# Kernel optimization log

Measured on AMD Instinct MI355X. Metric: run time of the kernel, lower is better.

The kernel has to match this reference:

```python
import jax, jax.numpy as jnp
import numpy as np

B, D, O = 512, 512, 512  # batch, indim, outdim

def setup_inputs() -> dict:
    key = jax.random.key(0)
    k1, k2, k3 = jax.random.split(key, 3)
    x = jax.random.normal(k1, (B, D), dtype=jnp.float32)
    mu_weight = jax.random.normal(k2, (O, D), dtype=jnp.float32) / np.sqrt(D)
    # inverse diagonal covariance entries (positive in spirit; uniform fill)
    inv_diag_C_weight = jax.random.uniform(k3, (O, D), dtype=jnp.float32)
    return {"x": x, "mu_weight": mu_weight, "inv_diag_C_weight": inv_diag_C_weight}

def reference(x, mu_weight, inv_diag_C_weight):
    # Original: logits = -(x-mu) @ diag(invC) @ (x-mu)^T per (batch, class) pair.
    # Diagonal structure => elementwise squared diff weighted by invC, summed over D.
    diff = x[:, None, :] - mu_weight[None, :, :]            # [B, O, D]
    logits = -jnp.einsum('bod,od->bo', diff * diff, inv_diag_C_weight)
    return logits                                            # [B, O]
```

## Files before the change

kernel.cpp:

```cpp
#include <hip/hip_runtime.h>

#define B_DIM 512
#define D_DIM 512
#define O_DIM 512
#define KSPLIT 8
#define DCHUNK 64


__global__ __launch_bounds__(256, 2)
void gda_main(const float* __restrict__ x,
              const float* __restrict__ mu,
              const float* __restrict__ ic,
              float* __restrict__ ws) {
    __shared__ float4 lds_x4[64 * 16];
    __shared__ float4 lds_ab4[64 * 16 * 2];
    __shared__ float  lds_cp[64 * 16];
    __shared__ float  lds_c[64];

    const int tid = threadIdx.x;
    const int bid = blockIdx.x;
    const int bb = bid & 7, ob = (bid >> 3) & 7, ks = bid >> 6;
    const int b0 = bb * 64, o0 = ob * 64, d0 = ks * DCHUNK;

    const int g   = tid & 15;
    const int row = tid >> 4;
#pragma unroll
    for (int i = 0; i < 4; ++i) {
        const int r = row + 16 * i;
        const int sw = g ^ (r & 7);
        const float4 xv = *(const float4*)&x [(b0 + r) * D_DIM + d0 + g * 4];
        lds_x4[r * 16 + sw] = xv;
        const float4 m4 = *(const float4*)&mu[(o0 + r) * D_DIM + d0 + g * 4];
        const float4 c4 = *(const float4*)&ic[(o0 + r) * D_DIM + d0 + g * 4];
        float4 a4, b4;
        a4.x = -c4.x;            a4.y = -c4.y;
        a4.z = -c4.z;            a4.w = -c4.w;
        b4.x = 2.0f * m4.x * c4.x; b4.y = 2.0f * m4.y * c4.y;
        b4.z = 2.0f * m4.z * c4.z; b4.w = 2.0f * m4.w * c4.w;
        lds_ab4[(r * 16 + sw) * 2 + 0] = a4;
        lds_ab4[(r * 16 + sw) * 2 + 1] = b4;
        lds_cp[r * 16 + g] = m4.x * m4.x * c4.x + m4.y * m4.y * c4.y
                           + m4.z * m4.z * c4.z + m4.w * m4.w * c4.w;
    }
    __syncthreads();

    if (tid < 64) {
        float s = 0.0f;
#pragma unroll
        for (int q = 0; q < 16; ++q) s += lds_cp[tid * 16 + q];
        lds_c[tid] = -s;
    }

    const int w    = tid >> 6;
    const int lane = tid & 63;
    const int cb   = lane >> 3;
    const int r8   = lane & 7;
    const int wb   = (w & 1) * 32, wo = (w >> 1) * 32;

    float acc[16];
#pragma unroll
    for (int q = 0; q < 16; ++q) acc[q] = 0.0f;

#pragma unroll
    for (int gg = 0; gg < 16; ++gg) {
        float4 xr[4], xs[4];
#pragma unroll
        for (int k = 0; k < 4; ++k) {
            xr[k] = lds_x4[(wb + cb + 8 * k) * 16 + (gg ^ cb)];
            xs[k].x = xr[k].x * xr[k].x;
            xs[k].y = xr[k].y * xr[k].y;
            xs[k].z = xr[k].z * xr[k].z;
            xs[k].w = xr[k].w * xr[k].w;
        }
#pragma unroll
        for (int j = 0; j < 4; ++j) {
            const int oo = wo + r8 + 8 * j;
            const float4 a4 = lds_ab4[(oo * 16 + (gg ^ r8)) * 2 + 0];
            const float4 b4 = lds_ab4[(oo * 16 + (gg ^ r8)) * 2 + 1];
#pragma unroll
            for (int k = 0; k < 4; ++k) {
                float t = acc[k * 4 + j];
                t = fmaf(a4.x, xs[k].x, t);  t = fmaf(b4.x, xr[k].x, t);
                t = fmaf(a4.y, xs[k].y, t);  t = fmaf(b4.y, xr[k].y, t);
                t = fmaf(a4.z, xs[k].z, t);  t = fmaf(b4.z, xr[k].z, t);
                t = fmaf(a4.w, xs[k].w, t);  t = fmaf(b4.w, xr[k].w, t);
                acc[k * 4 + j] = t;
            }
        }
    }
    __syncthreads();

    float* wsb = (float*)ws + (size_t)bid * 4096;
#pragma unroll
    for (int j = 0; j < 4; ++j) {
        const float cc = lds_c[wo + r8 + 8 * j];
#pragma unroll
        for (int k = 0; k < 4; ++k)
            wsb[(wb + cb + 8 * k) * 64 + (wo + r8 + 8 * j)] = acc[k * 4 + j] + cc;
    }
}

__global__ __launch_bounds__(256, 4)
void gda_reduce(const float* __restrict__ ws, float* __restrict__ out) {
    const int t0 = blockIdx.x * 1024 + threadIdx.x;
#pragma unroll
    for (int p = 0; p < 4; ++p) {
        const int flat = t0 + p * 256;
        const int b = flat >> 9, o = flat & 511;
        const int bb = b >> 6, bl = b & 63, ob = o >> 6, ol = o & 63;
        const float* base = ws + ((ob * 8 + bb) * 4096 + bl * 64 + ol);
        float s = 0.0f;
#pragma unroll
        for (int k = 0; k < KSPLIT; ++k) s += base[k * (64 * 4096)];
        out[flat] = s;
    }
}

extern "C" void kernel_launch(void* const* d_in, const int* in_sizes, int n_in,
                              void* d_out, int out_size, void* d_ws, size_t ws_size,
                              hipStream_t stream) {
    const float* x  = (const float*)d_in[0];
    const float* mu = (const float*)d_in[1];
    const float* ic = (const float*)d_in[2];
    float* ws  = (float*)d_ws;
    float* out = (float*)d_out;

    gda_main  <<<dim3(512), dim3(256), 0, stream>>>(x, mu, ic, ws);
    gda_reduce<<<dim3(256), dim3(256), 0, stream>>>(ws, out);
}
```

Measured before the change: 74.03 us.

## Use 128x64 tiles with 16-way K split, padded LDS and Horner FMA

Reshapes the main kernel to 128-row batch tiles with half-width D chunks and a 16-way K split. Each thread now holds 32 accumulators, which increases register reuse of the loaded mu/ic coefficients. The squared-x precompute is replaced with a Horner-form FMA pair, and XOR swizzling is replaced by padded LDS rows. The reduce kernel is vectorized with float4 loads, but workspace traffic doubles because of the larger split.

After: 76.51 us. 1.03x slower.

```diff
diff --git a/kernel.cpp b/kernel.cpp
--- a/kernel.cpp
+++ b/kernel.cpp
@@ -3,8 +3,8 @@
 #define B_DIM 512
 #define D_DIM 512
 #define O_DIM 512
-#define KSPLIT 8
-#define DCHUNK 64
+#define KSPLIT 16
+#define DCHUNK 32
 
 
 __global__ __launch_bounds__(256, 2)
@@ -12,42 +12,45 @@
               const float* __restrict__ mu,
               const float* __restrict__ ic,
               float* __restrict__ ws) {
-    __shared__ float4 lds_x4[64 * 16];
-    __shared__ float4 lds_ab4[64 * 16 * 2];
-    __shared__ float  lds_cp[64 * 16];
+    __shared__ float4 lds_x[128 * 9];
+    __shared__ float4 lds_a[64 * 9];
+    __shared__ float4 lds_b[64 * 9];
+    __shared__ float  lds_cp[64 * 9];
     __shared__ float  lds_c[64];
 
     const int tid = threadIdx.x;
     const int bid = blockIdx.x;
-    const int bb = bid & 7, ob = (bid >> 3) & 7, ks = bid >> 6;
-    const int b0 = bb * 64, o0 = ob * 64, d0 = ks * DCHUNK;
+    const int bb = bid & 3, ob = (bid >> 2) & 7, ks = bid >> 5;
+    const int b0 = bb * 128, o0 = ob * 64, d0 = ks * DCHUNK;
 
-    const int g   = tid & 15;
-    const int row = tid >> 4;
+    const int g   = tid & 7;
+    const int row = tid >> 3;
 #pragma unroll
     for (int i = 0; i < 4; ++i) {
-        const int r = row + 16 * i;
-        const int sw = g ^ (r & 7);
-        const float4 xv = *(const float4*)&x [(b0 + r) * D_DIM + d0 + g * 4];
-        lds_x4[r * 16 + sw] = xv;
+        const int r = row + 32 * i;
+        lds_x[r * 9 + g] = *(const float4*)&x[(b0 + r) * D_DIM + d0 + g * 4];
+    }
+#pragma unroll
+    for (int i = 0; i < 2; ++i) {
+        const int r = row + 32 * i;
         const float4 m4 = *(const float4*)&mu[(o0 + r) * D_DIM + d0 + g * 4];
         const float4 c4 = *(const float4*)&ic[(o0 + r) * D_DIM + d0 + g * 4];
         float4 a4, b4;
-        a4.x = -c4.x;            a4.y = -c4.y;
-        a4.z = -c4.z;            a4.w = -c4.w;
+        a4.x = -c4.x;              a4.y = -c4.y;
+        a4.z = -c4.z;              a4.w = -c4.w;
         b4.x = 2.0f * m4.x * c4.x; b4.y = 2.0f * m4.y * c4.y;
         b4.z = 2.0f * m4.z * c4.z; b4.w = 2.0f * m4.w * c4.w;
-        lds_ab4[(r * 16 + sw) * 2 + 0] = a4;
-        lds_ab4[(r * 16 + sw) * 2 + 1] = b4;
-        lds_cp[r * 16 + g] = m4.x * m4.x * c4.x + m4.y * m4.y * c4.y
-                           + m4.z * m4.z * c4.z + m4.w * m4.w * c4.w;
+        lds_a[r * 9 + g] = a4;
+        lds_b[r * 9 + g] = b4;
+        lds_cp[r * 9 + g] = m4.x * m4.x * c4.x + m4.y * m4.y * c4.y
+                          + m4.z * m4.z * c4.z + m4.w * m4.w * c4.w;
     }
     __syncthreads();
 
     if (tid < 64) {
         float s = 0.0f;
 #pragma unroll
-        for (int q = 0; q < 16; ++q) s += lds_cp[tid * 16 + q];
+        for (int q = 0; q < 8; ++q) s += lds_cp[tid * 9 + q];
         lds_c[tid] = -s;
     }
 
@@ -55,65 +58,64 @@
     const int lane = tid & 63;
     const int cb   = lane >> 3;
     const int r8   = lane & 7;
-    const int wb   = (w & 1) * 32, wo = (w >> 1) * 32;
+    const int wb   = (w & 1) * 64, wo = (w >> 1) * 32;
 
-    float acc[16];
+    const float4* xb = &lds_x[(wb + cb) * 9];
+    const float4* ap = &lds_a[(wo + r8) * 9];
+    const float4* bp = &lds_b[(wo + r8) * 9];
+
+    float acc[32];
 #pragma unroll
-    for (int q = 0; q < 16; ++q) acc[q] = 0.0f;
+    for (int q = 0; q < 32; ++q) acc[q] = 0.0f;
 
 #pragma unroll
-    for (int gg = 0; gg < 16; ++gg) {
-        float4 xr[4], xs[4];
+    for (int gg = 0; gg < 8; ++gg) {
+        float4 xr[8];
 #pragma unroll
-        for (int k = 0; k < 4; ++k) {
-            xr[k] = lds_x4[(wb + cb + 8 * k) * 16 + (gg ^ cb)];
-            xs[k].x = xr[k].x * xr[k].x;
-            xs[k].y = xr[k].y * xr[k].y;
-            xs[k].z = xr[k].z * xr[k].z;
-            xs[k].w = xr[k].w * xr[k].w;
-        }
+        for (int k = 0; k < 8; ++k) xr[k] = xb[k * 72 + gg];
 #pragma unroll
         for (int j = 0; j < 4; ++j) {
-            const int oo = wo + r8 + 8 * j;
-            const float4 a4 = lds_ab4[(oo * 16 + (gg ^ r8)) * 2 + 0];
-            const float4 b4 = lds_ab4[(oo * 16 + (gg ^ r8)) * 2 + 1];
+            const float4 a4 = ap[j * 72 + gg];
+            const float4 b4 = bp[j * 72 + gg];
 #pragma unroll
-            for (int k = 0; k < 4; ++k) {
+            for (int k = 0; k < 8; ++k) {
                 float t = acc[k * 4 + j];
-                t = fmaf(a4.x, xs[k].x, t);  t = fmaf(b4.x, xr[k].x, t);
-                t = fmaf(a4.y, xs[k].y, t);  t = fmaf(b4.y, xr[k].y, t);
-                t = fmaf(a4.z, xs[k].z, t);  t = fmaf(b4.z, xr[k].z, t);
-                t = fmaf(a4.w, xs[k].w, t);  t = fmaf(b4.w, xr[k].w, t);
+                float u;
+                u = fmaf(a4.x, xr[k].x, b4.x);  t = fmaf(u, xr[k].x, t);
+                u = fmaf(a4.y, xr[k].y, b4.y);  t = fmaf(u, xr[k].y, t);
+                u = fmaf(a4.z, xr[k].z, b4.z);  t = fmaf(u, xr[k].z, t);
+                u = fmaf(a4.w, xr[k].w, b4.w);  t = fmaf(u, xr[k].w, t);
                 acc[k * 4 + j] = t;
             }
         }
     }
     __syncthreads();
 
-    float* wsb = (float*)ws + (size_t)bid * 4096;
+    float* wsb = ws + (size_t)bid * 8192;
 #pragma unroll
     for (int j = 0; j < 4; ++j) {
         const float cc = lds_c[wo + r8 + 8 * j];
 #pragma unroll
-        for (int k = 0; k < 4; ++k)
+        for (int k = 0; k < 8; ++k)
             wsb[(wb + cb + 8 * k) * 64 + (wo + r8 + 8 * j)] = acc[k * 4 + j] + cc;
     }
 }
 
 __global__ __launch_bounds__(256, 4)
 void gda_reduce(const float* __restrict__ ws, float* __restrict__ out) {
-    const int t0 = blockIdx.x * 1024 + threadIdx.x;
+    const int fid = blockIdx.x * 256 + threadIdx.x;
+    const int b   = fid >> 7;
+    const int o4  = fid & 127;
+    const int ob  = o4 >> 4, ol4 = o4 & 15;
+    const int bbv = b >> 7, bl = b & 127;
+    const float* base = ws + ((bbv + 4 * ob) * 8192 + bl * 64 + ol4 * 4);
+    float4 s = {0.0f, 0.0f, 0.0f, 0.0f};
 #pragma unroll
-    for (int p = 0; p < 4; ++p) {
-        const int flat = t0 + p * 256;
-        const int b = flat >> 9, o = flat & 511;
-        const int bb = b >> 6, bl = b & 63, ob = o >> 6, ol = o & 63;
-        const float* base = ws + ((ob * 8 + bb) * 4096 + bl * 64 + ol);
-        float s = 0.0f;
-#pragma unroll
-        for (int k = 0; k < KSPLIT; ++k) s += base[k * (64 * 4096)];
-        out[flat] = s;
+    for (int k = 0; k < KSPLIT; ++k) {
+        const float4 v = *(const float4*)(base + (size_t)k * 262144);
+        s.x += v.x; s.y += v.y; s.z += v.z; s.w += v.w;
     }
+    ((float4*)out)[fid] = s;
 }
 
 extern "C" void kernel_launch(void* const* d_in, const int* in_sizes, int n_in,
```
